# Kernel optimization log

Hardware: AMD Instinct MI355X
Metric: run time of the kernel (lower is better)

Reference implementation:

```python
import jax, jax.numpy as jnp
import numpy as np

# Device / mapping constants (from iterator config in the original repo)
V_REF = 0.25
K_V = 2.0 * V_REF
G_MIN = 1e-5
G_MAX = 1e-3
N_AVG = 2.99
N_STD = 0.37
N_IN, N_OUT, BATCH = 1024, 512, 128


def setup_inputs() -> dict:
    key = jax.random.key(0)
    ks = jax.random.split(key, 6)
    x = jax.random.uniform(ks[0], (BATCH, N_IN), dtype=jnp.float32)
    stdv = 1.0 / np.sqrt(N_IN)
    w_pos = 0.5 + stdv * jax.random.normal(ks[1], (N_IN, N_OUT), dtype=jnp.float32)
    w_neg = 0.5 + stdv * jax.random.normal(ks[2], (N_IN, N_OUT), dtype=jnp.float32)
    b_pos = 0.5 * jnp.ones((N_OUT,), jnp.float32)
    b_neg = 0.5 * jnp.ones((N_OUT,), jnp.float32)
    # per-crosspoint I-V nonlinearity parameter n (n=2 means ohmic); clip below at 2
    n_devices = jnp.maximum(
        N_AVG + N_STD * jax.random.normal(ks[3], (N_IN + 1, 2 * N_OUT), dtype=jnp.float32),
        2.0,
    )
    return {"x": x, "w_pos": w_pos, "w_neg": w_neg, "b_pos": b_pos,
            "b_neg": b_neg, "n_devices": n_devices}


def reference(x, w_pos, w_neg, b_pos, b_neg, n_devices):
    B = x.shape[0]
    # append bias input of 1s -> [B, n_in+1]
    inputs = jnp.concatenate([x, jnp.ones((B, 1), x.dtype)], axis=1)
    # combined weights with bias row -> [n_in+1, n_out] each
    cw_pos = jnp.concatenate([w_pos, b_pos[None, :]], axis=0)
    cw_neg = jnp.concatenate([w_neg, b_neg[None, :]], axis=0)
    # interleave pos/neg columns -> [n_in+1, 2*n_out]
    combined = jnp.stack([cw_pos, cw_neg], axis=-1).reshape(cw_pos.shape[0], -1)
    # x -> V mapping
    V = K_V * inputs  # [B, n_in+1]
    # weight params -> conductances
    max_weight = jnp.max(jnp.abs(combined))
    k_G = (G_MAX - G_MIN) / max_weight
    G = k_G * jnp.abs(combined) + G_MIN  # [n_in+1, 2*n_out]
    # nonlinear I-V: I(V) = sign(V) * G*V_ref * (|V|/V_ref)^log2(n)
    exponent = jnp.log2(n_devices)          # [n_in+1, 2*n_out]
    sgn = jnp.sign(V)                       # [B, n_in+1]
    ratio = jnp.abs(V) / V_REF              # [B, n_in+1]
    I_ind = (sgn[:, :, None] * (G * V_REF)[None, :, :]
             * ratio[:, :, None] ** exponent[None, :, :])  # [B, n_in+1, 2*n_out]
    I = jnp.sum(I_ind, axis=1)              # [B, 2*n_out] (sum along bit lines)
    # differential pair currents -> output
    I_total = I[:, 0::2] - I[:, 1::2]       # [B, n_out]
    y = I_total / (K_V * k_G)
    return y
```

## Files before the change

kernel.cpp:

```cpp
#include <hip/hip_runtime.h>
#include <cstdint>
#include <cstddef>


#define B128 128
#define NIN  1024
#define NI   1025
#define NO   512
#define NJ   1024
#define GMIN 1.0e-5f
#define GSPAN (1.0e-3f - 1.0e-5f)
#define ZCH  8
#define CHUNK 128

__device__ __forceinline__ float flog2(float x) { return __builtin_amdgcn_logf(x); }
__device__ __forceinline__ float fexp2(float x) { return __builtin_amdgcn_exp2f(x); }

__global__ __launch_bounds__(1024) void k_prep(
    const float* __restrict__ x,
    const float* __restrict__ wp, const float* __restrict__ wn,
    const float* __restrict__ bp, const float* __restrict__ bn,
    float* __restrict__ LT, float* __restrict__ bmax, float* __restrict__ out)
{
    const int tid = blockIdx.x * 1024 + threadIdx.x;

    if (tid < B128 * NO) out[tid] = 0.0f;

    if (tid < NI * B128) {
        int i = tid >> 7, b = tid & 127;
        float xv = (i < NIN) ? x[b * NIN + i] : 1.0f;
        LT[tid] = 1.0f + flog2(xv);
    }

    float m = fmaxf(fmaxf(__builtin_fabsf(wp[tid]), __builtin_fabsf(wn[tid])),
                    fmaxf(__builtin_fabsf(wp[tid + 262144]), __builtin_fabsf(wn[tid + 262144])));
    if (tid < NO) m = fmaxf(m, fmaxf(__builtin_fabsf(bp[tid]), __builtin_fabsf(bn[tid])));

    __shared__ float red[16];
    #pragma unroll
    for (int off = 32; off > 0; off >>= 1) m = fmaxf(m, __shfl_down(m, off, 64));
    if ((threadIdx.x & 63) == 0) red[threadIdx.x >> 6] = m;
    __syncthreads();
    if (threadIdx.x < 16) {
        m = red[threadIdx.x];
        #pragma unroll
        for (int off = 8; off > 0; off >>= 1) m = fmaxf(m, __shfl_down(m, off, 16));
        if (threadIdx.x == 0) bmax[blockIdx.x] = m;
    }
}

__global__ __launch_bounds__(512) void k_main(
    const float* __restrict__ nd,
    const float* __restrict__ wp, const float* __restrict__ wn,
    const float* __restrict__ bp, const float* __restrict__ bn,
    const float* __restrict__ LT, const float* __restrict__ bmax,
    float* __restrict__ out)
{
    const int lane = threadIdx.x & 63;
    const int s    = threadIdx.x >> 6;
    const int o    = (blockIdx.x << 6) + lane;
    const int b0   = blockIdx.y << 4;

    float m = fmaxf(fmaxf(bmax[lane], bmax[lane + 64]),
                    fmaxf(bmax[lane + 128], bmax[lane + 192]));
    #pragma unroll
    for (int off = 32; off > 0; off >>= 1) m = fmaxf(m, __shfl_down(m, off, 64));
    const float maxw = __shfl(m, 0, 64);
    const float kG = GSPAN / maxw;
    const float C  = 0.5f * maxw / GSPAN;

    const int i0 = blockIdx.z * CHUNK + s;

    const float* pnd = nd + (size_t)i0 * NJ + 2 * o;
    const float* pwp = wp + (size_t)i0 * NO + o;
    const float* pwn = wn + (size_t)i0 * NO + o;
    const float* pL  = LT + (size_t)i0 * B128 + b0;

    float accp[16], accn[16];
    #pragma unroll
    for (int k = 0; k < 16; ++k) { accp[k] = 0.0f; accn[k] = 0.0f; }

    float2 nv = *(const float2*)pnd;
    float wvp = *pwp;
    float wvn = *pwn;
    float4 La = *(const float4*)(pL);
    float4 Lb = *(const float4*)(pL + 4);
    float4 Lc = *(const float4*)(pL + 8);
    float4 Ld = *(const float4*)(pL + 12);

    #pragma unroll 3
    for (int k = 0; k < 15; ++k) {
        pnd += 8 * NJ; pwp += 8 * NO; pwn += 8 * NO; pL += 8 * B128;
        float2 nv_n = *(const float2*)pnd;
        float wp_n = *pwp;
        float wn_n = *pwn;
        float4 Lan = *(const float4*)(pL);
        float4 Lbn = *(const float4*)(pL + 4);
        float4 Lcn = *(const float4*)(pL + 8);
        float4 Ldn = *(const float4*)(pL + 12);

        const float Ep = flog2(nv.x);
        const float En = flog2(nv.y);
        const float Wp = flog2(__builtin_fmaf(kG, __builtin_fabsf(wvp), GMIN));
        const float Wn = flog2(__builtin_fmaf(kG, __builtin_fabsf(wvn), GMIN));

        const float Lv[16] = {La.x, La.y, La.z, La.w, Lb.x, Lb.y, Lb.z, Lb.w,
                              Lc.x, Lc.y, Lc.z, Lc.w, Ld.x, Ld.y, Ld.z, Ld.w};
        #pragma unroll
        for (int j = 0; j < 16; ++j) {
            accp[j] += fexp2(__builtin_fmaf(Ep, Lv[j], Wp));
            accn[j] += fexp2(__builtin_fmaf(En, Lv[j], Wn));
        }

        nv = nv_n; wvp = wp_n; wvn = wn_n;
        La = Lan; Lb = Lbn; Lc = Lcn; Ld = Ldn;
    }

    {
        const float Ep = flog2(nv.x);
        const float En = flog2(nv.y);
        const float Wp = flog2(__builtin_fmaf(kG, __builtin_fabsf(wvp), GMIN));
        const float Wn = flog2(__builtin_fmaf(kG, __builtin_fabsf(wvn), GMIN));
        const float Lv[16] = {La.x, La.y, La.z, La.w, Lb.x, Lb.y, Lb.z, Lb.w,
                              Lc.x, Lc.y, Lc.z, Lc.w, Ld.x, Ld.y, Ld.z, Ld.w};
        #pragma unroll
        for (int j = 0; j < 16; ++j) {
            accp[j] += fexp2(__builtin_fmaf(Ep, Lv[j], Wp));
            accn[j] += fexp2(__builtin_fmaf(En, Lv[j], Wn));
        }
    }

    __shared__ float lds[8 * 64 * 33];
    {
        const int base = (s * 64 + lane) * 33;
        #pragma unroll
        for (int j = 0; j < 16; ++j) { lds[base + j] = accp[j]; lds[base + 16 + j] = accn[j]; }
    }
    __syncthreads();

    float bias = 0.0f;
    if (blockIdx.z == 0) {
        const float2 nb = *(const float2*)(nd + (size_t)NIN * NJ + 2 * o);
        const float gp = __builtin_fmaf(kG, __builtin_fabsf(bp[o]), GMIN);
        const float gn = __builtin_fmaf(kG, __builtin_fabsf(bn[o]), GMIN);
        bias = nb.x * gp - nb.y * gn;
    }

    {
        const int l = threadIdx.x & 63;
        #pragma unroll
        for (int r = 0; r < 2; ++r) {
            const int bb = (threadIdx.x >> 6) + (r << 3);
            float sum = bias;
            #pragma unroll
            for (int w = 0; w < 8; ++w) {
                const int base = (w * 64 + l) * 33;
                sum += lds[base + bb] - lds[base + 16 + bb];
            }
            unsafeAtomicAdd(out + (size_t)(b0 + bb) * NO + (blockIdx.x << 6) + l, C * sum);
        }
    }
}

extern "C" void kernel_launch(void* const* d_in, const int* in_sizes, int n_in,
                              void* d_out, int out_size, void* d_ws, size_t ws_size,
                              hipStream_t stream)
{
    const float* x  = (const float*)d_in[0];
    const float* wp = (const float*)d_in[1];
    const float* wn = (const float*)d_in[2];
    const float* bp = (const float*)d_in[3];
    const float* bn = (const float*)d_in[4];
    const float* nd = (const float*)d_in[5];
    float* out = (float*)d_out;

    unsigned char* ws = (unsigned char*)d_ws;
    float* bmax = (float*)ws;
    float* LT   = (float*)(ws + 4096);

    k_prep<<<256, 1024, 0, stream>>>(x, wp, wn, bp, bn, LT, bmax, out);
    k_main<<<dim3(8, 8, ZCH), 512, 0, stream>>>(nd, wp, wn, bp, bn, LT, bmax, out);
}
```

Before: 88.41 us.

## Precompute per-crosspoint log tables in separate kernel and fold output scale

Adds a k_tab kernel that computes log2(n) and log2 of the scaled conductance once per crosspoint, storing them as float4, and precomputes the bias term. The main kernel then streams this table instead of recomputing the logs for each of the 8 batch-tile blocks. The constant C is folded into the weight term, which removes the final multiply. This costs an extra launch and an 8 MB intermediate write and read, and it changes the load pattern to 16-byte loads with a two-deep prefetch.

```diff
diff --git a/kernel.cpp b/kernel.cpp
--- a/kernel.cpp
+++ b/kernel.cpp
@@ -49,86 +49,101 @@
     }
 }
 
-__global__ __launch_bounds__(512) void k_main(
+__global__ __launch_bounds__(512) void k_tab(
     const float* __restrict__ nd,
     const float* __restrict__ wp, const float* __restrict__ wn,
     const float* __restrict__ bp, const float* __restrict__ bn,
-    const float* __restrict__ LT, const float* __restrict__ bmax,
-    float* __restrict__ out)
+    const float* __restrict__ bmax,
+    float4* __restrict__ ew, float* __restrict__ biasv)
 {
+    const int i = blockIdx.x;
+    const int o = threadIdx.x;
     const int lane = threadIdx.x & 63;
-    const int s    = threadIdx.x >> 6;
-    const int o    = (blockIdx.x << 6) + lane;
-    const int b0   = blockIdx.y << 4;
 
     float m = fmaxf(fmaxf(bmax[lane], bmax[lane + 64]),
                     fmaxf(bmax[lane + 128], bmax[lane + 192]));
     #pragma unroll
     for (int off = 32; off > 0; off >>= 1) m = fmaxf(m, __shfl_down(m, off, 64));
     const float maxw = __shfl(m, 0, 64);
-    const float kG = GSPAN / maxw;
-    const float C  = 0.5f * maxw / GSPAN;
+    const float hdelta = 0.5f * (maxw * (GMIN / GSPAN));
 
-    const int i0 = blockIdx.z * CHUNK + s;
+    const float2 nv = *(const float2*)(nd + (size_t)i * NJ + 2 * o);
+    if (i < NIN) {
+        const float wvp = __builtin_fabsf(wp[(size_t)i * NO + o]);
+        const float wvn = __builtin_fabsf(wn[(size_t)i * NO + o]);
+        ew[(size_t)i * NO + o] = make_float4(
+            flog2(nv.x), flog2(nv.y),
+            flog2(__builtin_fmaf(0.5f, wvp, hdelta)),
+            flog2(__builtin_fmaf(0.5f, wvn, hdelta)));
+    } else {
+        const float gp = __builtin_fmaf(0.5f, __builtin_fabsf(bp[o]), hdelta);
+        const float gn = __builtin_fmaf(0.5f, __builtin_fabsf(bn[o]), hdelta);
+        biasv[o] = nv.x * gp - nv.y * gn;
+    }
+}
 
-    const float* pnd = nd + (size_t)i0 * NJ + 2 * o;
-    const float* pwp = wp + (size_t)i0 * NO + o;
-    const float* pwn = wn + (size_t)i0 * NO + o;
-    const float* pL  = LT + (size_t)i0 * B128 + b0;
+__global__ __launch_bounds__(512) void k_main(
+    const float4* __restrict__ ew, const float* __restrict__ LT,
+    const float* __restrict__ biasv, float* __restrict__ out)
+{
+    const int lane = threadIdx.x & 63;
+    const int s    = threadIdx.x >> 6;
+    const int o    = (blockIdx.x << 6) + lane;
+    const int b0   = blockIdx.y << 4;
+    const int i0   = blockIdx.z * CHUNK + s;
+
+    const float4* pEW = ew + (size_t)i0 * NO + o;
+    const float*  pL  = LT + (size_t)i0 * B128 + b0;
 
     float accp[16], accn[16];
     #pragma unroll
     for (int k = 0; k < 16; ++k) { accp[k] = 0.0f; accn[k] = 0.0f; }
 
-    float2 nv = *(const float2*)pnd;
-    float wvp = *pwp;
-    float wvn = *pwn;
+    float4 e0 = pEW[0];
+    float4 e1 = pEW[8 * NO];
+    const float4* pE = pEW + 16 * NO;
     float4 La = *(const float4*)(pL);
     float4 Lb = *(const float4*)(pL + 4);
     float4 Lc = *(const float4*)(pL + 8);
     float4 Ld = *(const float4*)(pL + 12);
 
-    #pragma unroll 3
-    for (int k = 0; k < 15; ++k) {
-        pnd += 8 * NJ; pwp += 8 * NO; pwn += 8 * NO; pL += 8 * B128;
-        float2 nv_n = *(const float2*)pnd;
-        float wp_n = *pwp;
-        float wn_n = *pwn;
-        float4 Lan = *(const float4*)(pL);
-        float4 Lbn = *(const float4*)(pL + 4);
-        float4 Lcn = *(const float4*)(pL + 8);
-        float4 Ldn = *(const float4*)(pL + 12);
+#define STEP(E) do { \
+        const float Lv[16] = {La.x, La.y, La.z, La.w, Lb.x, Lb.y, Lb.z, Lb.w, \
+                              Lc.x, Lc.y, Lc.z, Lc.w, Ld.x, Ld.y, Ld.z, Ld.w}; \
+        _Pragma("unroll") \
+        for (int j = 0; j < 16; ++j) { \
+            accp[j] += fexp2(__builtin_fmaf((E).x, Lv[j], (E).z)); \
+            accn[j] += fexp2(__builtin_fmaf((E).y, Lv[j], (E).w)); \
+        } \
+    } while (0)
 
-        const float Ep = flog2(nv.x);
-        const float En = flog2(nv.y);
-        const float Wp = flog2(__builtin_fmaf(kG, __builtin_fabsf(wvp), GMIN));
-        const float Wn = flog2(__builtin_fmaf(kG, __builtin_fabsf(wvn), GMIN));
+    #pragma unroll 2
+    for (int k = 0; k < 14; ++k) {
+        const float4 e2 = *pE;
+        pE += 8 * NO;
+        pL += 8 * B128;
+        const float4 Lan = *(const float4*)(pL);
+        const float4 Lbn = *(const float4*)(pL + 4);
+        const float4 Lcn = *(const float4*)(pL + 8);
+        const float4 Ldn = *(const float4*)(pL + 12);
 
-        const float Lv[16] = {La.x, La.y, La.z, La.w, Lb.x, Lb.y, Lb.z, Lb.w,
-                              Lc.x, Lc.y, Lc.z, Lc.w, Ld.x, Ld.y, Ld.z, Ld.w};
-        #pragma unroll
-        for (int j = 0; j < 16; ++j) {
-            accp[j] += fexp2(__builtin_fmaf(Ep, Lv[j], Wp));
-            accn[j] += fexp2(__builtin_fmaf(En, Lv[j], Wn));
-        }
+        STEP(e0);
 
-        nv = nv_n; wvp = wp_n; wvn = wn_n;
+        e0 = e1; e1 = e2;
         La = Lan; Lb = Lbn; Lc = Lcn; Ld = Ldn;
     }
-
     {
-        const float Ep = flog2(nv.x);
-        const float En = flog2(nv.y);
-        const float Wp = flog2(__builtin_fmaf(kG, __builtin_fabsf(wvp), GMIN));
-        const float Wn = flog2(__builtin_fmaf(kG, __builtin_fabsf(wvn), GMIN));
-        const float Lv[16] = {La.x, La.y, La.z, La.w, Lb.x, Lb.y, Lb.z, Lb.w,
-                              Lc.x, Lc.y, Lc.z, Lc.w, Ld.x, Ld.y, Ld.z, Ld.w};
-        #pragma unroll
-        for (int j = 0; j < 16; ++j) {
-            accp[j] += fexp2(__builtin_fmaf(Ep, Lv[j], Wp));
-            accn[j] += fexp2(__builtin_fmaf(En, Lv[j], Wn));
-        }
+        pL += 8 * B128;
+        const float4 Lan = *(const float4*)(pL);
+        const float4 Lbn = *(const float4*)(pL + 4);
+        const float4 Lcn = *(const float4*)(pL + 8);
+        const float4 Ldn = *(const float4*)(pL + 12);
+        STEP(e0);
+        e0 = e1;
+        La = Lan; Lb = Lbn; Lc = Lcn; Ld = Ldn;
     }
+    STEP(e0);
+#undef STEP
 
     __shared__ float lds[8 * 64 * 33];
     {
@@ -139,12 +154,7 @@
     __syncthreads();
 
     float bias = 0.0f;
-    if (blockIdx.z == 0) {
-        const float2 nb = *(const float2*)(nd + (size_t)NIN * NJ + 2 * o);
-        const float gp = __builtin_fmaf(kG, __builtin_fabsf(bp[o]), GMIN);
-        const float gn = __builtin_fmaf(kG, __builtin_fabsf(bn[o]), GMIN);
-        bias = nb.x * gp - nb.y * gn;
-    }
+    if (blockIdx.z == 0) bias = biasv[o];
 
     {
         const int l = threadIdx.x & 63;
@@ -157,7 +167,7 @@
                 const int base = (w * 64 + l) * 33;
                 sum += lds[base + bb] - lds[base + 16 + bb];
             }
-            unsafeAtomicAdd(out + (size_t)(b0 + bb) * NO + (blockIdx.x << 6) + l, C * sum);
+            unsafeAtomicAdd(out + (size_t)(b0 + bb) * NO + (blockIdx.x << 6) + l, sum);
         }
     }
 }
@@ -175,9 +185,12 @@
     float* out = (float*)d_out;
 
     unsigned char* ws = (unsigned char*)d_ws;
-    float* bmax = (float*)ws;
-    float* LT   = (float*)(ws + 4096);
+    float*  bmax  = (float*)ws;
+    float*  LT    = (float*)(ws + 4096);
+    float4* EW    = (float4*)(ws + 528896);
+    float*  biasv = (float*)(ws + 8917504);
 
     k_prep<<<256, 1024, 0, stream>>>(x, wp, wn, bp, bn, LT, bmax, out);
-    k_main<<<dim3(8, 8, ZCH), 512, 0, stream>>>(nd, wp, wn, bp, bn, LT, bmax, out);
+    k_tab<<<NI, 512, 0, stream>>>(nd, wp, wn, bp, bn, bmax, EW, biasv);
+    k_main<<<dim3(8, 8, ZCH), 512, 0, stream>>>(EW, LT, biasv, out);
 }
```

New measurement: 92.35 us. 4.5% more time.
